# Kernel tuning notes

Measured on AMD Instinct MI355X. Metric: run time of the kernel, lower is better.

The kernel has to match this reference:

```python
import jax, jax.numpy as jnp
import numpy as np

EPS = 1e-12  # torch F.normalize eps


def setup_inputs() -> dict:
    key = jax.random.key(0)
    k1, k2, k3 = jax.random.split(key, 3)
    N, D, L = 8192, 768, 24576
    x = jax.random.normal(k1, (N, D), dtype=jnp.float32)
    # paper init: row-normalized gaussian rows of shape [latent_dim, input_dim]
    w = jax.random.normal(k2, (L, D), dtype=jnp.float32)
    enc_w = w / jnp.maximum(jnp.linalg.norm(w, axis=1, keepdims=True), EPS)
    enc_b = jax.random.normal(k3, (L,), dtype=jnp.float32) * 0.01
    pre_bias = jnp.zeros((D,), dtype=jnp.float32)
    return {"x": x, "enc_w": enc_w, "enc_b": enc_b, "pre_bias": pre_bias, "k": 32}


def _topk_mask(latents, k):
    # keep values >= k-th largest per row (ties kept, as in the torch code)
    vals, _ = jax.lax.top_k(latents, k)            # [N, k]
    thresh = vals[:, -1:]                          # [N, 1]
    return latents * (latents >= thresh)


def reference(x, enc_w, enc_b, pre_bias, k):
    # norm_input: subtract pre_bias then L2-normalize rows
    xc = x - pre_bias
    xn = xc / jnp.maximum(jnp.linalg.norm(xc, axis=1, keepdims=True), EPS)
    latents = xn @ enc_w.T + enc_b                 # [N, L]
    sparse = _topk_mask(latents, k)                # [N, L], ~k nonzeros/row
    # tied decoder: F.linear(sparse, enc_w.t()) == sparse @ enc_w
    out = sparse @ enc_w + pre_bias                # [N, D]
    return out, sparse
```

## Files before the change

### kernel.cpp

```cpp
#include <hip/hip_runtime.h>
#include <hip/hip_bf16.h>
#include <stdint.h>

#define N_ROWS 8192
#define DIM    768
#define LAT    24576
#define KSEL   32

using bf16x8 = __attribute__((ext_vector_type(8))) short;
using f32x4  = __attribute__((ext_vector_type(4))) float;

__device__ __forceinline__ unsigned short f2bf(float f) {
  unsigned int b = __float_as_uint(f);
  return (unsigned short)((b + 0x7FFFu + ((b >> 16) & 1u)) >> 16);
}
__device__ __forceinline__ float bf2f(unsigned short u) {
  return __uint_as_float(((unsigned int)u) << 16);
}
__device__ __forceinline__ unsigned int mapf(float f) {
  unsigned int u = __float_as_uint(f);
  return (u & 0x80000000u) ? ~u : (u | 0x80000000u);
}

__global__ __launch_bounds__(192) void k_norm(const float* __restrict__ x,
                                              const float* __restrict__ pre_bias,
                                              float* __restrict__ xn,
                                              unsigned short* __restrict__ xnbf) {
  const int row = blockIdx.x;
  const int t   = threadIdx.x;
  float4 xc = *(const float4*)&x[(size_t)row * DIM + t * 4];
  float4 pb = *(const float4*)&pre_bias[t * 4];
  xc.x -= pb.x; xc.y -= pb.y; xc.z -= pb.z; xc.w -= pb.w;
  double ss = (double)xc.x * xc.x + (double)xc.y * xc.y
            + (double)xc.z * xc.z + (double)xc.w * xc.w;
  #pragma unroll
  for (int off = 32; off; off >>= 1) ss += __shfl_down(ss, off);
  __shared__ double wsum[3];
  if ((t & 63) == 0) wsum[t >> 6] = ss;
  __syncthreads();
  const double tot = wsum[0] + wsum[1] + wsum[2];
  const float nrm = (float)fmax(sqrt(tot), 1e-12);
  float4 o;
  o.x = xc.x / nrm; o.y = xc.y / nrm; o.z = xc.z / nrm; o.w = xc.w / nrm;
  *(float4*)&xn[(size_t)row * DIM + t * 4] = o;
  if (xnbf) {
    ushort4 h;
    h.x = f2bf(o.x); h.y = f2bf(o.y); h.z = f2bf(o.z); h.w = f2bf(o.w);
    *(ushort4*)&xnbf[(size_t)row * DIM + t * 4] = h;
  }
}

__global__ __launch_bounds__(256) void k_cvt(const float* __restrict__ W,
                                             unsigned short* __restrict__ Wbf) {
  const int n4 = LAT * DIM / 4;
  const int stride = gridDim.x * blockDim.x;
  for (int i = blockIdx.x * blockDim.x + threadIdx.x; i < n4; i += stride) {
    float4 v = *(const float4*)&W[(size_t)i * 4];
    ushort4 h;
    h.x = f2bf(v.x); h.y = f2bf(v.y); h.z = f2bf(v.z); h.w = f2bf(v.w);
    *(ushort4*)&Wbf[(size_t)i * 4] = h;
  }
}

__global__ __launch_bounds__(256) void k_gemm_bf16(const unsigned short* __restrict__ A,
                                                   const unsigned short* __restrict__ B,
                                                   const float* __restrict__ bias,
                                                   unsigned short* __restrict__ C) {
  __shared__ __align__(16) unsigned short Al[2][128 * 32];
  __shared__ __align__(16) unsigned short Bl[2][128 * 32];
  const int tid  = threadIdx.x;
  const int lane = tid & 63;
  const int wave = tid >> 6;
  const int bm = blockIdx.y * 128;
  const int bn = blockIdx.x * 128;
  const int wr = (wave >> 1) * 64;
  const int wc = (wave & 1) * 64;
  const int fr = lane & 15;
  const int fq = lane >> 4;
  const int r0 = tid >> 2;
  const int c0 = tid & 3;

  f32x4 acc[4][4];
  #pragma unroll
  for (int m = 0; m < 4; ++m)
    #pragma unroll
    for (int n = 0; n < 4; ++n) acc[m][n] = (f32x4){0.f, 0.f, 0.f, 0.f};

  uint4 ra0, ra1, rb0, rb1;
  ra0 = *(const uint4*)&A[(size_t)(bm + r0) * DIM + c0 * 8];
  ra1 = *(const uint4*)&A[(size_t)(bm + 64 + r0) * DIM + c0 * 8];
  rb0 = *(const uint4*)&B[(size_t)(bn + r0) * DIM + c0 * 8];
  rb1 = *(const uint4*)&B[(size_t)(bn + 64 + r0) * DIM + c0 * 8];
  *(uint4*)&Al[0][r0 * 32 + c0 * 8]        = ra0;
  *(uint4*)&Al[0][(64 + r0) * 32 + c0 * 8] = ra1;
  *(uint4*)&Bl[0][r0 * 32 + c0 * 8]        = rb0;
  *(uint4*)&Bl[0][(64 + r0) * 32 + c0 * 8] = rb1;

  const int NT = DIM / 32;
  for (int kt = 0; kt < NT; ++kt) {
    const int buf = kt & 1;
    __syncthreads();
    if (kt + 1 < NT) {
      const int k0 = (kt + 1) * 32;
      ra0 = *(const uint4*)&A[(size_t)(bm + r0) * DIM + k0 + c0 * 8];
      ra1 = *(const uint4*)&A[(size_t)(bm + 64 + r0) * DIM + k0 + c0 * 8];
      rb0 = *(const uint4*)&B[(size_t)(bn + r0) * DIM + k0 + c0 * 8];
      rb1 = *(const uint4*)&B[(size_t)(bn + 64 + r0) * DIM + k0 + c0 * 8];
    }
    bf16x8 af[4], bfr[4];
    #pragma unroll
    for (int m = 0; m < 4; ++m)
      af[m] = *(const bf16x8*)&Al[buf][(wr + m * 16 + fr) * 32 + fq * 8];
    #pragma unroll
    for (int n = 0; n < 4; ++n)
      bfr[n] = *(const bf16x8*)&Bl[buf][(wc + n * 16 + fr) * 32 + fq * 8];
    #pragma unroll
    for (int m = 0; m < 4; ++m)
      #pragma unroll
      for (int n = 0; n < 4; ++n)
        acc[m][n] = __builtin_amdgcn_mfma_f32_16x16x32_bf16(af[m], bfr[n], acc[m][n], 0, 0, 0);
    if (kt + 1 < NT) {
      const int wb = buf ^ 1;
      *(uint4*)&Al[wb][r0 * 32 + c0 * 8]        = ra0;
      *(uint4*)&Al[wb][(64 + r0) * 32 + c0 * 8] = ra1;
      *(uint4*)&Bl[wb][r0 * 32 + c0 * 8]        = rb0;
      *(uint4*)&Bl[wb][(64 + r0) * 32 + c0 * 8] = rb1;
    }
  }

  #pragma unroll
  for (int n = 0; n < 4; ++n) {
    const int col = bn + wc + n * 16 + fr;
    const float bv = bias[col];
    #pragma unroll
    for (int m = 0; m < 4; ++m) {
      #pragma unroll
      for (int j = 0; j < 4; ++j) {
        const int row = bm + wr + m * 16 + fq * 4 + j;
        C[(size_t)row * LAT + col] = f2bf(acc[m][n][j] + bv);
      }
    }
  }
}

#define NBINS 8192
#define MARGIN 8e-3f
#define CCAP 192

__global__ __launch_bounds__(512) void k_screen(const unsigned short* __restrict__ S,
                                                int* __restrict__ cand_idx,
                                                int* __restrict__ cand_cnt) {
  const int row = blockIdx.x;
  const int t   = threadIdx.x;
  const unsigned short* rp = S + (size_t)row * LAT;

  float v[48];
  #pragma unroll
  for (int i = 0; i < 12; ++i) {
    ushort4 h = *(const ushort4*)&rp[(i * 512 + t) * 4];
    v[i * 4 + 0] = bf2f(h.x); v[i * 4 + 1] = bf2f(h.y);
    v[i * 4 + 2] = bf2f(h.z); v[i * 4 + 3] = bf2f(h.w);
  }

  __shared__ unsigned int hist[NBINS];
  __shared__ unsigned int csum[512];
  __shared__ unsigned int sh_chunk, sh_rchunk, sh_thru;
  __shared__ int sh_nc;
  if (t == 0) sh_nc = 0;
  #pragma unroll
  for (int i = 0; i < NBINS / 512; ++i) hist[t + i * 512] = 0u;
  __syncthreads();

  #pragma unroll
  for (int i = 0; i < 48; ++i) atomicAdd(&hist[mapf(v[i]) >> 19], 1u);
  __syncthreads();

  unsigned int cs = 0;
  #pragma unroll
  for (int i = 0; i < 16; ++i) cs += hist[t * 16 + i];
  csum[t] = cs;
  __syncthreads();
  for (int off = 1; off < 512; off <<= 1) {
    unsigned int add = (t + off < 512) ? csum[t + off] : 0u;
    __syncthreads();
    csum[t] += add;
    __syncthreads();
  }
  {
    const unsigned int nxt = (t + 1 < 512) ? csum[t + 1] : 0u;
    if (csum[t] >= KSEL && nxt < KSEL) { sh_chunk = (unsigned)t; sh_rchunk = nxt; }
  }
  __syncthreads();
  if (t == 0) {
    const unsigned int c0 = sh_chunk * 16u;
    unsigned int cum = sh_rchunk;
    unsigned int bin = c0;
    for (int b = 15; b >= 0; --b) {
      const unsigned int h = hist[c0 + b];
      if (cum + h >= KSEL) { bin = c0 + b; break; }
      cum += h;
    }
    const unsigned int lo = bin << 19;
    const unsigned int orig = (lo & 0x80000000u) ? (lo & 0x7FFFFFFFu) : ~lo;
    const float L = __uint_as_float(orig);
    sh_thru = mapf(L - MARGIN);
  }
  __syncthreads();
  const unsigned int thru = sh_thru;

  #pragma unroll
  for (int i = 0; i < 48; ++i) {
    if (mapf(v[i]) >= thru) {
      int p = atomicAdd(&sh_nc, 1);
      if (p < CCAP) cand_idx[row * CCAP + p] = ((i >> 2) * 512 + t) * 4 + (i & 3);
    }
  }
  __syncthreads();
  if (t == 0) cand_cnt[row] = (sh_nc < CCAP) ? sh_nc : CCAP;
}

__global__ __launch_bounds__(256) void k_rescore_seq(const float* __restrict__ xn,
                                                     const float* __restrict__ W,
                                                     const float* __restrict__ bias,
                                                     const int* __restrict__ cand_idx,
                                                     const int* __restrict__ cand_cnt,
                                                     float* __restrict__ tk_val,
                                                     int* __restrict__ tk_idx,
                                                     int* __restrict__ tk_cnt) {
  const int row = blockIdx.x;
  const int t   = threadIdx.x;
  const int cnt = cand_cnt[row];

  __shared__ float xs[DIM];
  __shared__ float rv[CCAP];
  __shared__ unsigned int sh_t;
  __shared__ int sh_kc;
  if (t == 0) sh_kc = 0;
  if (t < 192) *(float4*)&xs[t * 4] = *(const float4*)&xn[(size_t)row * DIM + t * 4];
  __syncthreads();

  if (t < cnt) {
    const int idx = cand_idx[row * CCAP + t];
    const float* wp = &W[(size_t)idx * DIM];
    float acc = 0.0f;
    for (int k4 = 0; k4 < DIM / 4; ++k4) {
      const float4 wv = *(const float4*)&wp[k4 * 4];
      acc = fmaf(xs[k4 * 4 + 0], wv.x, acc);
      acc = fmaf(xs[k4 * 4 + 1], wv.y, acc);
      acc = fmaf(xs[k4 * 4 + 2], wv.z, acc);
      acc = fmaf(xs[k4 * 4 + 3], wv.w, acc);
    }
    rv[t] = acc + bias[idx];
  }
  __syncthreads();

  if (t < cnt) {
    const unsigned int uj = mapf(rv[t]);
    unsigned int g = 0, ge = 0;
    for (int i = 0; i < cnt; ++i) {
      const unsigned int ui = mapf(rv[i]);
      g  += (ui >  uj);
      ge += (ui >= uj);
    }
    if (g < KSEL && ge >= KSEL) sh_t = uj;
  }
  __syncthreads();
  if (t < cnt) {
    const float val = rv[t];
    if (mapf(val) >= sh_t) {
      int p = atomicAdd(&sh_kc, 1);
      if (p < 64) { tk_val[row * 64 + p] = val; tk_idx[row * 64 + p] = cand_idx[row * CCAP + t]; }
    }
  }
  __syncthreads();
  if (t == 0) tk_cnt[row] = (sh_kc < 64) ? sh_kc : 64;
}

__global__ __launch_bounds__(256) void k_scatter(const float* __restrict__ tk_val,
                                                 const int* __restrict__ tk_idx,
                                                 const int* __restrict__ tk_cnt,
                                                 float* __restrict__ sparse) {
  const int row = blockIdx.x;
  const int t   = threadIdx.x;
  float* rp = sparse + (size_t)row * LAT;
  const float4 z = {0.f, 0.f, 0.f, 0.f};
  #pragma unroll
  for (int i = 0; i < LAT / (256 * 4); ++i) *(float4*)&rp[(i * 256 + t) * 4] = z;
  __syncthreads();
  if (t < tk_cnt[row]) rp[tk_idx[row * 64 + t]] = tk_val[row * 64 + t];
}

__global__ __launch_bounds__(192) void k_dec(const float* __restrict__ tk_val,
                                             const int* __restrict__ tk_idx,
                                             const int* __restrict__ tk_cnt,
                                             const float* __restrict__ W,
                                             const float* __restrict__ pre_bias,
                                             float* __restrict__ out) {
  const int row = blockIdx.x;
  const int t   = threadIdx.x;
  const int cnt = tk_cnt[row];
  float4 acc = *(const float4*)&pre_bias[t * 4];
  for (int e = 0; e < cnt; ++e) {
    const float val = tk_val[row * 64 + e];
    const int   idx = tk_idx[row * 64 + e];
    const float4 w = *(const float4*)&W[(size_t)idx * DIM + t * 4];
    acc.x = fmaf(val, w.x, acc.x);
    acc.y = fmaf(val, w.y, acc.y);
    acc.z = fmaf(val, w.z, acc.z);
    acc.w = fmaf(val, w.w, acc.w);
  }
  *(float4*)&out[(size_t)row * DIM + t * 4] = acc;
}

#define BM 128
#define BN 128
#define BK 32
#define PAD 4

__global__ __launch_bounds__(256) void k_gemm(const float* __restrict__ A,
                                              const float* __restrict__ B,
                                              const float* __restrict__ bias,
                                              float* __restrict__ C) {
  __shared__ float As[BK][BM + PAD];
  __shared__ float Bs[BK][BN + PAD];
  const int tid = threadIdx.x;
  const int bm = blockIdx.y * BM;
  const int bn = blockIdx.x * BN;
  const int tx = tid & 15;
  const int ty = tid >> 4;
  const int kq = tid & 7;
  const int rr = tid >> 3;

  float acc[8][8];
  #pragma unroll
  for (int i = 0; i < 8; ++i)
    #pragma unroll
    for (int j = 0; j < 8; ++j) acc[i][j] = 0.0f;

  float4 va[4], vb[4];
  #pragma unroll
  for (int i = 0; i < 4; ++i) {
    const int row = rr + 32 * i;
    va[i] = *(const float4*)&A[(size_t)(bm + row) * DIM + kq * 4];
    vb[i] = *(const float4*)&B[(size_t)(bn + row) * DIM + kq * 4];
  }

  for (int k0 = 0; k0 < DIM; k0 += BK) {
    #pragma unroll
    for (int i = 0; i < 4; ++i) {
      const int row = rr + 32 * i;
      As[kq * 4 + 0][row] = va[i].x; As[kq * 4 + 1][row] = va[i].y;
      As[kq * 4 + 2][row] = va[i].z; As[kq * 4 + 3][row] = va[i].w;
      Bs[kq * 4 + 0][row] = vb[i].x; Bs[kq * 4 + 1][row] = vb[i].y;
      Bs[kq * 4 + 2][row] = vb[i].z; Bs[kq * 4 + 3][row] = vb[i].w;
    }
    __syncthreads();
    if (k0 + BK < DIM) {
      #pragma unroll
      for (int i = 0; i < 4; ++i) {
        const int row = rr + 32 * i;
        va[i] = *(const float4*)&A[(size_t)(bm + row) * DIM + (k0 + BK) + kq * 4];
        vb[i] = *(const float4*)&B[(size_t)(bn + row) * DIM + (k0 + BK) + kq * 4];
      }
    }
    #pragma unroll
    for (int k = 0; k < BK; ++k) {
      float a[8], b[8];
      *(float4*)&b[0] = *(const float4*)&Bs[k][tx * 4];
      *(float4*)&b[4] = *(const float4*)&Bs[k][64 + tx * 4];
      *(float4*)&a[0] = *(const float4*)&As[k][ty * 8];
      *(float4*)&a[4] = *(const float4*)&As[k][ty * 8 + 4];
      #pragma unroll
      for (int i = 0; i < 8; ++i)
        #pragma unroll
        for (int j = 0; j < 8; ++j)
          acc[i][j] = fmaf(a[i], b[j], acc[i][j]);
    }
    __syncthreads();
  }

  const float4 b0 = *(const float4*)&bias[bn + tx * 4];
  const float4 b1 = *(const float4*)&bias[bn + 64 + tx * 4];
  #pragma unroll
  for (int i = 0; i < 8; ++i) {
    const size_t m = (size_t)(bm + ty * 8 + i);
    float4 v0, v1;
    v0.x = acc[i][0] + b0.x; v0.y = acc[i][1] + b0.y;
    v0.z = acc[i][2] + b0.z; v0.w = acc[i][3] + b0.w;
    v1.x = acc[i][4] + b1.x; v1.y = acc[i][5] + b1.y;
    v1.z = acc[i][6] + b1.z; v1.w = acc[i][7] + b1.w;
    *(float4*)&C[m * LAT + bn + tx * 4]      = v0;
    *(float4*)&C[m * LAT + bn + 64 + tx * 4] = v1;
  }
}

#define TPB_TK 512
#define CAND_CAP 512

template <int EMIT>
__global__ __launch_bounds__(TPB_TK) void k_topk(float* __restrict__ lat,
                                                 float* __restrict__ tk_val,
                                                 int* __restrict__ tk_idx,
                                                 int* __restrict__ tk_cnt) {
  const int row = blockIdx.x;
  const int t   = threadIdx.x;
  float* rowp = lat + (size_t)row * LAT;

  float4 v[12];
  #pragma unroll
  for (int i = 0; i < 12; ++i) v[i] = *(const float4*)&rowp[(i * TPB_TK + t) * 4];

  __shared__ unsigned int hist[NBINS];
  __shared__ unsigned int csum[TPB_TK];
  __shared__ unsigned int cand[CAND_CAP];
  __shared__ int sh_nc, sh_kc;
  __shared__ unsigned int sh_bin, sh_need, sh_thresh, sh_rchunk, sh_chunk;

  if (t == 0) { sh_nc = 0; sh_kc = 0; }
  #pragma unroll
  for (int i = 0; i < NBINS / TPB_TK; ++i) hist[t + i * TPB_TK] = 0u;
  __syncthreads();

  #pragma unroll
  for (int i = 0; i < 12; ++i) {
    atomicAdd(&hist[mapf(v[i].x) >> 19], 1u);
    atomicAdd(&hist[mapf(v[i].y) >> 19], 1u);
    atomicAdd(&hist[mapf(v[i].z) >> 19], 1u);
    atomicAdd(&hist[mapf(v[i].w) >> 19], 1u);
  }
  __syncthreads();

  unsigned int cs = 0;
  #pragma unroll
  for (int i = 0; i < 16; ++i) cs += hist[t * 16 + i];
  csum[t] = cs;
  __syncthreads();
  for (int off = 1; off < TPB_TK; off <<= 1) {
    unsigned int add = (t + off < TPB_TK) ? csum[t + off] : 0u;
    __syncthreads();
    csum[t] += add;
    __syncthreads();
  }
  {
    const unsigned int nxt = (t + 1 < TPB_TK) ? csum[t + 1] : 0u;
    if (csum[t] >= KSEL && nxt < KSEL) { sh_chunk = (unsigned)t; sh_rchunk = nxt; }
  }
  __syncthreads();
  if (t == 0) {
    const unsigned int c0 = sh_chunk * 16u;
    unsigned int cum = sh_rchunk;
    for (int b = 15; b >= 0; --b) {
      const unsigned int h = hist[c0 + b];
      if (cum + h >= KSEL) { sh_bin = c0 + b; sh_need = KSEL - cum; break; }
      cum += h;
    }
  }
  __syncthreads();
  const unsigned int bstar = sh_bin;

  #pragma unroll
  for (int i = 0; i < 12; ++i) {
    unsigned int u;
    u = mapf(v[i].x); if ((u >> 19) == bstar) { int p = atomicAdd(&sh_nc, 1); if (p < CAND_CAP) cand[p] = u; }
    u = mapf(v[i].y); if ((u >> 19) == bstar) { int p = atomicAdd(&sh_nc, 1); if (p < CAND_CAP) cand[p] = u; }
    u = mapf(v[i].z); if ((u >> 19) == bstar) { int p = atomicAdd(&sh_nc, 1); if (p < CAND_CAP) cand[p] = u; }
    u = mapf(v[i].w); if ((u >> 19) == bstar) { int p = atomicAdd(&sh_nc, 1); if (p < CAND_CAP) cand[p] = u; }
  }
  __syncthreads();
  const int nc = (sh_nc < CAND_CAP) ? sh_nc : CAND_CAP;
  const unsigned int need = sh_need;
  for (int j = t; j < nc; j += TPB_TK) {
    const unsigned int uj = cand[j];
    unsigned int g = 0, ge = 0;
    for (int i = 0; i < nc; ++i) {
      g  += (cand[i] >  uj);
      ge += (cand[i] >= uj);
    }
    if (g < need && ge >= need) sh_thresh = uj;
  }
  __syncthreads();
  const unsigned int tu = sh_thresh;

  #pragma unroll
  for (int i = 0; i < 12; ++i) {
    const int base = (i * TPB_TK + t) * 4;
    float4 o = v[i];
    unsigned int u;
    u = mapf(o.x); if (u >= tu) { if (EMIT) { int p = atomicAdd(&sh_kc, 1); if (p < 64) { tk_val[row * 64 + p] = o.x; tk_idx[row * 64 + p] = base + 0; } } } else o.x = 0.0f;
    u = mapf(o.y); if (u >= tu) { if (EMIT) { int p = atomicAdd(&sh_kc, 1); if (p < 64) { tk_val[row * 64 + p] = o.y; tk_idx[row * 64 + p] = base + 1; } } } else o.y = 0.0f;
    u = mapf(o.z); if (u >= tu) { if (EMIT) { int p = atomicAdd(&sh_kc, 1); if (p < 64) { tk_val[row * 64 + p] = o.z; tk_idx[row * 64 + p] = base + 2; } } } else o.z = 0.0f;
    u = mapf(o.w); if (u >= tu) { if (EMIT) { int p = atomicAdd(&sh_kc, 1); if (p < 64) { tk_val[row * 64 + p] = o.w; tk_idx[row * 64 + p] = base + 3; } } } else o.w = 0.0f;
    *(float4*)&rowp[base] = o;
  }
  if (EMIT) {
    __syncthreads();
    if (t == 0) tk_cnt[row] = (sh_kc < 64) ? sh_kc : 64;
  }
}

__global__ __launch_bounds__(256) void k_dec_scan(const float* __restrict__ sparse,
                                                  const float* __restrict__ W,
                                                  const float* __restrict__ pre_bias,
                                                  float* __restrict__ out) {
  const int row = blockIdx.x;
  const int t   = threadIdx.x;
  const float* rowp = sparse + (size_t)row * LAT;

  __shared__ float sval[96];
  __shared__ int   sidx[96];
  __shared__ int   scnt;
  if (t == 0) scnt = 0;
  __syncthreads();

  #pragma unroll
  for (int i = 0; i < LAT / (256 * 4); ++i) {
    const int base = (i * 256 + t) * 4;
    const float4 v = *(const float4*)&rowp[base];
    if (v.x != 0.0f) { int p = atomicAdd(&scnt, 1); if (p < 96) { sval[p] = v.x; sidx[p] = base + 0; } }
    if (v.y != 0.0f) { int p = atomicAdd(&scnt, 1); if (p < 96) { sval[p] = v.y; sidx[p] = base + 1; } }
    if (v.z != 0.0f) { int p = atomicAdd(&scnt, 1); if (p < 96) { sval[p] = v.z; sidx[p] = base + 2; } }
    if (v.w != 0.0f) { int p = atomicAdd(&scnt, 1); if (p < 96) { sval[p] = v.w; sidx[p] = base + 3; } }
  }
  __syncthreads();
  const int cnt = (scnt < 96) ? scnt : 96;

  if (t < 192) {
    float4 acc = *(const float4*)&pre_bias[t * 4];
    for (int e = 0; e < cnt; ++e) {
      const float val = sval[e];
      const float4 w = *(const float4*)&W[(size_t)sidx[e] * DIM + t * 4];
      acc.x = fmaf(val, w.x, acc.x);
      acc.y = fmaf(val, w.y, acc.y);
      acc.z = fmaf(val, w.z, acc.z);
      acc.w = fmaf(val, w.w, acc.w);
    }
    *(float4*)&out[(size_t)row * DIM + t * 4] = acc;
  }
}

extern "C" void kernel_launch(void* const* d_in, const int* in_sizes, int n_in,
                              void* d_out, int out_size, void* d_ws, size_t ws_size,
                              hipStream_t stream) {
  const float* x        = (const float*)d_in[0];
  const float* enc_w    = (const float*)d_in[1];
  const float* enc_b    = (const float*)d_in[2];
  const float* pre_bias = (const float*)d_in[3];

  float* out    = (float*)d_out;
  float* sparse = (float*)d_out + (size_t)N_ROWS * DIM;
  float* xn     = out;

  char* spb = (char*)sparse;
  unsigned short* xnbf   = (unsigned short*)spb;
  unsigned short* wbf    = (unsigned short*)(spb + (size_t)N_ROWS * DIM * 2);
  unsigned short* screen = (unsigned short*)(sparse + (size_t)N_ROWS * LAT / 2);

  char* wsb = (char*)d_ws;
  size_t off = 0;
  int*   cand_idx = (int*)(wsb + off); off += (size_t)N_ROWS * CCAP * 4;
  int*   cand_cnt = (int*)(wsb + off); off += (size_t)N_ROWS * 4;
  float* tk_val   = (float*)(wsb + off); off += (size_t)N_ROWS * 64 * 4;
  int*   tk_idx   = (int*)(wsb + off); off += (size_t)N_ROWS * 64 * 4;
  int*   tk_cnt   = (int*)(wsb + off); off += (size_t)N_ROWS * 4;
  const bool fast = ws_size >= off;

  if (fast) {
    k_norm<<<N_ROWS, 192, 0, stream>>>(x, pre_bias, xn, xnbf);
    k_cvt<<<2048, 256, 0, stream>>>(enc_w, wbf);
    dim3 ggrid(LAT / 128, N_ROWS / 128);
    k_gemm_bf16<<<ggrid, 256, 0, stream>>>(xnbf, wbf, enc_b, screen);
    k_screen<<<N_ROWS, 512, 0, stream>>>(screen, cand_idx, cand_cnt);
    k_rescore_seq<<<N_ROWS, 256, 0, stream>>>(xn, enc_w, enc_b, cand_idx, cand_cnt,
                                              tk_val, tk_idx, tk_cnt);
    k_scatter<<<N_ROWS, 256, 0, stream>>>(tk_val, tk_idx, tk_cnt, sparse);
    k_dec<<<N_ROWS, 192, 0, stream>>>(tk_val, tk_idx, tk_cnt, enc_w, pre_bias, out);
  } else {
    const size_t ws_small = (size_t)N_ROWS * 64 * 4 * 2 + (size_t)N_ROWS * 4;
    const bool use_lists = ws_size >= ws_small;
    float* f_val = (float*)d_ws;
    int*   f_idx = (int*)(f_val + (size_t)N_ROWS * 64);
    int*   f_cnt = f_idx + (size_t)N_ROWS * 64;

    k_norm<<<N_ROWS, 192, 0, stream>>>(x, pre_bias, xn, nullptr);
    dim3 ggrid(LAT / BN, N_ROWS / BM);
    k_gemm<<<ggrid, 256, 0, stream>>>(xn, enc_w, enc_b, sparse);
    if (use_lists) {
      k_topk<1><<<N_ROWS, TPB_TK, 0, stream>>>(sparse, f_val, f_idx, f_cnt);
      k_dec<<<N_ROWS, 192, 0, stream>>>(f_val, f_idx, f_cnt, enc_w, pre_bias, out);
    } else {
      k_topk<0><<<N_ROWS, TPB_TK, 0, stream>>>(sparse, nullptr, nullptr, nullptr);
      k_dec_scan<<<N_ROWS, 256, 0, stream>>>(sparse, enc_w, pre_bias, out);
    }
  }
}
```

Before: 1.797 ms.

## Use direct global-to-LDS loads in bf16 GEMM and fuse scatter with decoder

The bf16 screening GEMM now stages tiles with global_load_lds, which writes global data straight into LDS and skips the register round trip and explicit LDS stores. Each wave loads two 16-row segments, laid out so the LDS layout matches the old one. Separately, the scatter and decoder kernels are merged into one launch per row, saving a kernel launch and a reread of the top-k lists. The fp32 GEMM and top-k kernels are only moved within the file. The GEMM keeps a single barrier per iteration with no explicit wait on the async LDS loads, which could risk a race.

Result: no change. 1.810 ms (+0.7%).

```diff
diff --git a/kernel.cpp b/kernel.cpp
--- a/kernel.cpp
+++ b/kernel.cpp
@@ -20,6 +20,13 @@
 __device__ __forceinline__ unsigned int mapf(float f) {
   unsigned int u = __float_as_uint(f);
   return (u & 0x80000000u) ? ~u : (u | 0x80000000u);
+}
+
+__device__ __forceinline__ void gload16(const unsigned short* g, unsigned short* l) {
+  __builtin_amdgcn_global_load_lds(
+      (const __attribute__((address_space(1))) unsigned int*)(uintptr_t)g,
+      (__attribute__((address_space(3))) unsigned int*)(unsigned int)(uintptr_t)l,
+      16, 0, 0);
 }
 
 __global__ __launch_bounds__(192) void k_norm(const float* __restrict__ x,
@@ -77,8 +84,15 @@
   const int wc = (wave & 1) * 64;
   const int fr = lane & 15;
   const int fq = lane >> 4;
-  const int r0 = tid >> 2;
-  const int c0 = tid & 3;
+
+  const int seg0 = wave * 2;
+  const int rseg = lane >> 2;
+  const int ch   = lane & 3;
+
+  const unsigned short* gA0 = &A[(size_t)(bm + 16 * seg0 +      rseg) * DIM + ch * 8];
+  const unsigned short* gA1 = &A[(size_t)(bm + 16 * seg0 + 16 + rseg) * DIM + ch * 8];
+  const unsigned short* gB0 = &B[(size_t)(bn + 16 * seg0 +      rseg) * DIM + ch * 8];
+  const unsigned short* gB1 = &B[(size_t)(bn + 16 * seg0 + 16 + rseg) * DIM + ch * 8];
 
   f32x4 acc[4][4];
   #pragma unroll
@@ -86,27 +100,21 @@
     #pragma unroll
     for (int n = 0; n < 4; ++n) acc[m][n] = (f32x4){0.f, 0.f, 0.f, 0.f};
 
-  uint4 ra0, ra1, rb0, rb1;
-  ra0 = *(const uint4*)&A[(size_t)(bm + r0) * DIM + c0 * 8];
-  ra1 = *(const uint4*)&A[(size_t)(bm + 64 + r0) * DIM + c0 * 8];
-  rb0 = *(const uint4*)&B[(size_t)(bn + r0) * DIM + c0 * 8];
-  rb1 = *(const uint4*)&B[(size_t)(bn + 64 + r0) * DIM + c0 * 8];
-  *(uint4*)&Al[0][r0 * 32 + c0 * 8]        = ra0;
-  *(uint4*)&Al[0][(64 + r0) * 32 + c0 * 8] = ra1;
-  *(uint4*)&Bl[0][r0 * 32 + c0 * 8]        = rb0;
-  *(uint4*)&Bl[0][(64 + r0) * 32 + c0 * 8] = rb1;
+#define STAGE(buf, k0)                                            \
+  do {                                                            \
+    gload16(gA0 + (k0), &Al[buf][(seg0)     * 512]);              \
+    gload16(gA1 + (k0), &Al[buf][(seg0 + 1) * 512]);              \
+    gload16(gB0 + (k0), &Bl[buf][(seg0)     * 512]);              \
+    gload16(gB1 + (k0), &Bl[buf][(seg0 + 1) * 512]);              \
+  } while (0)
+
+  STAGE(0, 0);
 
   const int NT = DIM / 32;
   for (int kt = 0; kt < NT; ++kt) {
     const int buf = kt & 1;
     __syncthreads();
-    if (kt + 1 < NT) {
-      const int k0 = (kt + 1) * 32;
-      ra0 = *(const uint4*)&A[(size_t)(bm + r0) * DIM + k0 + c0 * 8];
-      ra1 = *(const uint4*)&A[(size_t)(bm + 64 + r0) * DIM + k0 + c0 * 8];
-      rb0 = *(const uint4*)&B[(size_t)(bn + r0) * DIM + k0 + c0 * 8];
-      rb1 = *(const uint4*)&B[(size_t)(bn + 64 + r0) * DIM + k0 + c0 * 8];
-    }
+    if (kt + 1 < NT) STAGE(buf ^ 1, (kt + 1) * 32);
     bf16x8 af[4], bfr[4];
     #pragma unroll
     for (int m = 0; m < 4; ++m)
@@ -119,14 +127,8 @@
       #pragma unroll
       for (int n = 0; n < 4; ++n)
         acc[m][n] = __builtin_amdgcn_mfma_f32_16x16x32_bf16(af[m], bfr[n], acc[m][n], 0, 0, 0);
-    if (kt + 1 < NT) {
-      const int wb = buf ^ 1;
-      *(uint4*)&Al[wb][r0 * 32 + c0 * 8]        = ra0;
-      *(uint4*)&Al[wb][(64 + r0) * 32 + c0 * 8] = ra1;
-      *(uint4*)&Bl[wb][r0 * 32 + c0 * 8]        = rb0;
-      *(uint4*)&Bl[wb][(64 + r0) * 32 + c0 * 8] = rb1;
-    }
-  }
+  }
+#undef STAGE
 
   #pragma unroll
   for (int n = 0; n < 4; ++n) {
@@ -276,10 +278,13 @@
   if (t == 0) tk_cnt[row] = (sh_kc < 64) ? sh_kc : 64;
 }
 
-__global__ __launch_bounds__(256) void k_scatter(const float* __restrict__ tk_val,
-                                                 const int* __restrict__ tk_idx,
-                                                 const int* __restrict__ tk_cnt,
-                                                 float* __restrict__ sparse) {
+__global__ __launch_bounds__(256) void k_scatter_dec(const float* __restrict__ tk_val,
+                                                     const int* __restrict__ tk_idx,
+                                                     const int* __restrict__ tk_cnt,
+                                                     const float* __restrict__ W,
+                                                     const float* __restrict__ pre_bias,
+                                                     float* __restrict__ sparse,
+                                                     float* __restrict__ out) {
   const int row = blockIdx.x;
   const int t   = threadIdx.x;
   float* rp = sparse + (size_t)row * LAT;
@@ -287,7 +292,207 @@
   #pragma unroll
   for (int i = 0; i < LAT / (256 * 4); ++i) *(float4*)&rp[(i * 256 + t) * 4] = z;
   __syncthreads();
-  if (t < tk_cnt[row]) rp[tk_idx[row * 64 + t]] = tk_val[row * 64 + t];
+  const int cnt = tk_cnt[row];
+  if (t < cnt) rp[tk_idx[row * 64 + t]] = tk_val[row * 64 + t];
+  if (t < 192) {
+    float4 acc = *(const float4*)&pre_bias[t * 4];
+    for (int e = 0; e < cnt; ++e) {
+      const float val = tk_val[row * 64 + e];
+      const int   idx = tk_idx[row * 64 + e];
+      const float4 w = *(const float4*)&W[(size_t)idx * DIM + t * 4];
+      acc.x = fmaf(val, w.x, acc.x);
+      acc.y = fmaf(val, w.y, acc.y);
+      acc.z = fmaf(val, w.z, acc.z);
+      acc.w = fmaf(val, w.w, acc.w);
+    }
+    *(float4*)&out[(size_t)row * DIM + t * 4] = acc;
+  }
+}
+
+#define BM 128
+#define BN 128
+#define BK 32
+#define PAD 4
+
+__global__ __launch_bounds__(256) void k_gemm(const float* __restrict__ A,
+                                              const float* __restrict__ B,
+                                              const float* __restrict__ bias,
+                                              float* __restrict__ C) {
+  __shared__ float As[BK][BM + PAD];
+  __shared__ float Bs[BK][BN + PAD];
+  const int tid = threadIdx.x;
+  const int bm = blockIdx.y * BM;
+  const int bn = blockIdx.x * BN;
+  const int tx = tid & 15;
+  const int ty = tid >> 4;
+  const int kq = tid & 7;
+  const int rr = tid >> 3;
+
+  float acc[8][8];
+  #pragma unroll
+  for (int i = 0; i < 8; ++i)
+    #pragma unroll
+    for (int j = 0; j < 8; ++j) acc[i][j] = 0.0f;
+
+  float4 va[4], vb[4];
+  #pragma unroll
+  for (int i = 0; i < 4; ++i) {
+    const int row = rr + 32 * i;
+    va[i] = *(const float4*)&A[(size_t)(bm + row) * DIM + kq * 4];
+    vb[i] = *(const float4*)&B[(size_t)(bn + row) * DIM + kq * 4];
+  }
+
+  for (int k0 = 0; k0 < DIM; k0 += BK) {
+    #pragma unroll
+    for (int i = 0; i < 4; ++i) {
+      const int row = rr + 32 * i;
+      As[kq * 4 + 0][row] = va[i].x; As[kq * 4 + 1][row] = va[i].y;
+      As[kq * 4 + 2][row] = va[i].z; As[kq * 4 + 3][row] = va[i].w;
+      Bs[kq * 4 + 0][row] = vb[i].x; Bs[kq * 4 + 1][row] = vb[i].y;
+      Bs[kq * 4 + 2][row] = vb[i].z; Bs[kq * 4 + 3][row] = vb[i].w;
+    }
+    __syncthreads();
+    if (k0 + BK < DIM) {
+      #pragma unroll
+      for (int i = 0; i < 4; ++i) {
+        const int row = rr + 32 * i;
+        va[i] = *(const float4*)&A[(size_t)(bm + row) * DIM + (k0 + BK) + kq * 4];
+        vb[i] = *(const float4*)&B[(size_t)(bn + row) * DIM + (k0 + BK) + kq * 4];
+      }
+    }
+    #pragma unroll
+    for (int k = 0; k < BK; ++k) {
+      float a[8], b[8];
+      *(float4*)&b[0] = *(const float4*)&Bs[k][tx * 4];
+      *(float4*)&b[4] = *(const float4*)&Bs[k][64 + tx * 4];
+      *(float4*)&a[0] = *(const float4*)&As[k][ty * 8];
+      *(float4*)&a[4] = *(const float4*)&As[k][ty * 8 + 4];
+      #pragma unroll
+      for (int i = 0; i < 8; ++i)
+        #pragma unroll
+        for (int j = 0; j < 8; ++j)
+          acc[i][j] = fmaf(a[i], b[j], acc[i][j]);
+    }
+    __syncthreads();
+  }
+
+  const float4 b0 = *(const float4*)&bias[bn + tx * 4];
+  const float4 b1 = *(const float4*)&bias[bn + 64 + tx * 4];
+  #pragma unroll
+  for (int i = 0; i < 8; ++i) {
+    const size_t m = (size_t)(bm + ty * 8 + i);
+    float4 v0, v1;
+    v0.x = acc[i][0] + b0.x; v0.y = acc[i][1] + b0.y;
+    v0.z = acc[i][2] + b0.z; v0.w = acc[i][3] + b0.w;
+    v1.x = acc[i][4] + b1.x; v1.y = acc[i][5] + b1.y;
+    v1.z = acc[i][6] + b1.z; v1.w = acc[i][7] + b1.w;
+    *(float4*)&C[m * LAT + bn + tx * 4]      = v0;
+    *(float4*)&C[m * LAT + bn + 64 + tx * 4] = v1;
+  }
+}
+
+#define TPB_TK 512
+#define CAND_CAP 512
+
+template <int EMIT>
+__global__ __launch_bounds__(TPB_TK) void k_topk(float* __restrict__ lat,
+                                                 float* __restrict__ tk_val,
+                                                 int* __restrict__ tk_idx,
+                                                 int* __restrict__ tk_cnt) {
+  const int row = blockIdx.x;
+  const int t   = threadIdx.x;
+  float* rowp = lat + (size_t)row * LAT;
+
+  float4 v[12];
+  #pragma unroll
+  for (int i = 0; i < 12; ++i) v[i] = *(const float4*)&rowp[(i * TPB_TK + t) * 4];
+
+  __shared__ unsigned int hist[NBINS];
+  __shared__ unsigned int csum[TPB_TK];
+  __shared__ unsigned int cand[CAND_CAP];
+  __shared__ int sh_nc, sh_kc;
+  __shared__ unsigned int sh_bin, sh_need, sh_thresh, sh_rchunk, sh_chunk;
+
+  if (t == 0) { sh_nc = 0; sh_kc = 0; }
+  #pragma unroll
+  for (int i = 0; i < NBINS / TPB_TK; ++i) hist[t + i * TPB_TK] = 0u;
+  __syncthreads();
+
+  #pragma unroll
+  for (int i = 0; i < 12; ++i) {
+    atomicAdd(&hist[mapf(v[i].x) >> 19], 1u);
+    atomicAdd(&hist[mapf(v[i].y) >> 19], 1u);
+    atomicAdd(&hist[mapf(v[i].z) >> 19], 1u);
+    atomicAdd(&hist[mapf(v[i].w) >> 19], 1u);
+  }
+  __syncthreads();
+
+  unsigned int cs = 0;
+  #pragma unroll
+  for (int i = 0; i < 16; ++i) cs += hist[t * 16 + i];
+  csum[t] = cs;
+  __syncthreads();
+  for (int off = 1; off < TPB_TK; off <<= 1) {
+    unsigned int add = (t + off < TPB_TK) ? csum[t + off] : 0u;
+    __syncthreads();
+    csum[t] += add;
+    __syncthreads();
+  }
+  {
+    const unsigned int nxt = (t + 1 < TPB_TK) ? csum[t + 1] : 0u;
+    if (csum[t] >= KSEL && nxt < KSEL) { sh_chunk = (unsigned)t; sh_rchunk = nxt; }
+  }
+  __syncthreads();
+  if (t == 0) {
+    const unsigned int c0 = sh_chunk * 16u;
+    unsigned int cum = sh_rchunk;
+    for (int b = 15; b >= 0; --b) {
+      const unsigned int h = hist[c0 + b];
+      if (cum + h >= KSEL) { sh_bin = c0 + b; sh_need = KSEL - cum; break; }
+      cum += h;
+    }
+  }
+  __syncthreads();
+  const unsigned int bstar = sh_bin;
+
+  #pragma unroll
+  for (int i = 0; i < 12; ++i) {
+    unsigned int u;
+    u = mapf(v[i].x); if ((u >> 19) == bstar) { int p = atomicAdd(&sh_nc, 1); if (p < CAND_CAP) cand[p] = u; }
+    u = mapf(v[i].y); if ((u >> 19) == bstar) { int p = atomicAdd(&sh_nc, 1); if (p < CAND_CAP) cand[p] = u; }
+    u = mapf(v[i].z); if ((u >> 19) == bstar) { int p = atomicAdd(&sh_nc, 1); if (p < CAND_CAP) cand[p] = u; }
+    u = mapf(v[i].w); if ((u >> 19) == bstar) { int p = atomicAdd(&sh_nc, 1); if (p < CAND_CAP) cand[p] = u; }
+  }
+  __syncthreads();
+  const int nc = (sh_nc < CAND_CAP) ? sh_nc : CAND_CAP;
+  const unsigned int need = sh_need;
+  for (int j = t; j < nc; j += TPB_TK) {
+    const unsigned int uj = cand[j];
+    unsigned int g = 0, ge = 0;
+    for (int i = 0; i < nc; ++i) {
+      g  += (cand[i] >  uj);
+      ge += (cand[i] >= uj);
+    }
+    if (g < need && ge >= need) sh_thresh = uj;
+  }
+  __syncthreads();
+  const unsigned int tu = sh_thresh;
+
+  #pragma unroll
+  for (int i = 0; i < 12; ++i) {
+    const int base = (i * TPB_TK + t) * 4;
+    float4 o = v[i];
+    unsigned int u;
+    u = mapf(o.x); if (u >= tu) { if (EMIT) { int p = atomicAdd(&sh_kc, 1); if (p < 64) { tk_val[row * 64 + p] = o.x; tk_idx[row * 64 + p] = base + 0; } } } else o.x = 0.0f;
+    u = mapf(o.y); if (u >= tu) { if (EMIT) { int p = atomicAdd(&sh_kc, 1); if (p < 64) { tk_val[row * 64 + p] = o.y; tk_idx[row * 64 + p] = base + 1; } } } else o.y = 0.0f;
+    u = mapf(o.z); if (u >= tu) { if (EMIT) { int p = atomicAdd(&sh_kc, 1); if (p < 64) { tk_val[row * 64 + p] = o.z; tk_idx[row * 64 + p] = base + 2; } } } else o.z = 0.0f;
+    u = mapf(o.w); if (u >= tu) { if (EMIT) { int p = atomicAdd(&sh_kc, 1); if (p < 64) { tk_val[row * 64 + p] = o.w; tk_idx[row * 64 + p] = base + 3; } } } else o.w = 0.0f;
+    *(float4*)&rowp[base] = o;
+  }
+  if (EMIT) {
+    __syncthreads();
+    if (t == 0) tk_cnt[row] = (sh_kc < 64) ? sh_kc : 64;
+  }
 }
 
 __global__ __launch_bounds__(192) void k_dec(const float* __restrict__ tk_val,
@@ -312,192 +517,6 @@
   *(float4*)&out[(size_t)row * DIM + t * 4] = acc;
 }
 
-#define BM 128
-#define BN 128
-#define BK 32
-#define PAD 4
-
-__global__ __launch_bounds__(256) void k_gemm(const float* __restrict__ A,
-                                              const float* __restrict__ B,
-                                              const float* __restrict__ bias,
-                                              float* __restrict__ C) {
-  __shared__ float As[BK][BM + PAD];
-  __shared__ float Bs[BK][BN + PAD];
-  const int tid = threadIdx.x;
-  const int bm = blockIdx.y * BM;
-  const int bn = blockIdx.x * BN;
-  const int tx = tid & 15;
-  const int ty = tid >> 4;
-  const int kq = tid & 7;
-  const int rr = tid >> 3;
-
-  float acc[8][8];
-  #pragma unroll
-  for (int i = 0; i < 8; ++i)
-    #pragma unroll
-    for (int j = 0; j < 8; ++j) acc[i][j] = 0.0f;
-
-  float4 va[4], vb[4];
-  #pragma unroll
-  for (int i = 0; i < 4; ++i) {
-    const int row = rr + 32 * i;
-    va[i] = *(const float4*)&A[(size_t)(bm + row) * DIM + kq * 4];
-    vb[i] = *(const float4*)&B[(size_t)(bn + row) * DIM + kq * 4];
-  }
-
-  for (int k0 = 0; k0 < DIM; k0 += BK) {
-    #pragma unroll
-    for (int i = 0; i < 4; ++i) {
-      const int row = rr + 32 * i;
-      As[kq * 4 + 0][row] = va[i].x; As[kq * 4 + 1][row] = va[i].y;
-      As[kq * 4 + 2][row] = va[i].z; As[kq * 4 + 3][row] = va[i].w;
-      Bs[kq * 4 + 0][row] = vb[i].x; Bs[kq * 4 + 1][row] = vb[i].y;
-      Bs[kq * 4 + 2][row] = vb[i].z; Bs[kq * 4 + 3][row] = vb[i].w;
-    }
-    __syncthreads();
-    if (k0 + BK < DIM) {
-      #pragma unroll
-      for (int i = 0; i < 4; ++i) {
-        const int row = rr + 32 * i;
-        va[i] = *(const float4*)&A[(size_t)(bm + row) * DIM + (k0 + BK) + kq * 4];
-        vb[i] = *(const float4*)&B[(size_t)(bn + row) * DIM + (k0 + BK) + kq * 4];
-      }
-    }
-    #pragma unroll
-    for (int k = 0; k < BK; ++k) {
-      float a[8], b[8];
-      *(float4*)&b[0] = *(const float4*)&Bs[k][tx * 4];
-      *(float4*)&b[4] = *(const float4*)&Bs[k][64 + tx * 4];
-      *(float4*)&a[0] = *(const float4*)&As[k][ty * 8];
-      *(float4*)&a[4] = *(const float4*)&As[k][ty * 8 + 4];
-      #pragma unroll
-      for (int i = 0; i < 8; ++i)
-        #pragma unroll
-        for (int j = 0; j < 8; ++j)
-          acc[i][j] = fmaf(a[i], b[j], acc[i][j]);
-    }
-    __syncthreads();
-  }
-
-  const float4 b0 = *(const float4*)&bias[bn + tx * 4];
-  const float4 b1 = *(const float4*)&bias[bn + 64 + tx * 4];
-  #pragma unroll
-  for (int i = 0; i < 8; ++i) {
-    const size_t m = (size_t)(bm + ty * 8 + i);
-    float4 v0, v1;
-    v0.x = acc[i][0] + b0.x; v0.y = acc[i][1] + b0.y;
-    v0.z = acc[i][2] + b0.z; v0.w = acc[i][3] + b0.w;
-    v1.x = acc[i][4] + b1.x; v1.y = acc[i][5] + b1.y;
-    v1.z = acc[i][6] + b1.z; v1.w = acc[i][7] + b1.w;
-    *(float4*)&C[m * LAT + bn + tx * 4]      = v0;
-    *(float4*)&C[m * LAT + bn + 64 + tx * 4] = v1;
-  }
-}
-
-#define TPB_TK 512
-#define CAND_CAP 512
-
-template <int EMIT>
-__global__ __launch_bounds__(TPB_TK) void k_topk(float* __restrict__ lat,
-                                                 float* __restrict__ tk_val,
-                                                 int* __restrict__ tk_idx,
-                                                 int* __restrict__ tk_cnt) {
-  const int row = blockIdx.x;
-  const int t   = threadIdx.x;
-  float* rowp = lat + (size_t)row * LAT;
-
-  float4 v[12];
-  #pragma unroll
-  for (int i = 0; i < 12; ++i) v[i] = *(const float4*)&rowp[(i * TPB_TK + t) * 4];
-
-  __shared__ unsigned int hist[NBINS];
-  __shared__ unsigned int csum[TPB_TK];
-  __shared__ unsigned int cand[CAND_CAP];
-  __shared__ int sh_nc, sh_kc;
-  __shared__ unsigned int sh_bin, sh_need, sh_thresh, sh_rchunk, sh_chunk;
-
-  if (t == 0) { sh_nc = 0; sh_kc = 0; }
-  #pragma unroll
-  for (int i = 0; i < NBINS / TPB_TK; ++i) hist[t + i * TPB_TK] = 0u;
-  __syncthreads();
-
-  #pragma unroll
-  for (int i = 0; i < 12; ++i) {
-    atomicAdd(&hist[mapf(v[i].x) >> 19], 1u);
-    atomicAdd(&hist[mapf(v[i].y) >> 19], 1u);
-    atomicAdd(&hist[mapf(v[i].z) >> 19], 1u);
-    atomicAdd(&hist[mapf(v[i].w) >> 19], 1u);
-  }
-  __syncthreads();
-
-  unsigned int cs = 0;
-  #pragma unroll
-  for (int i = 0; i < 16; ++i) cs += hist[t * 16 + i];
-  csum[t] = cs;
-  __syncthreads();
-  for (int off = 1; off < TPB_TK; off <<= 1) {
-    unsigned int add = (t + off < TPB_TK) ? csum[t + off] : 0u;
-    __syncthreads();
-    csum[t] += add;
-    __syncthreads();
-  }
-  {
-    const unsigned int nxt = (t + 1 < TPB_TK) ? csum[t + 1] : 0u;
-    if (csum[t] >= KSEL && nxt < KSEL) { sh_chunk = (unsigned)t; sh_rchunk = nxt; }
-  }
-  __syncthreads();
-  if (t == 0) {
-    const unsigned int c0 = sh_chunk * 16u;
-    unsigned int cum = sh_rchunk;
-    for (int b = 15; b >= 0; --b) {
-      const unsigned int h = hist[c0 + b];
-      if (cum + h >= KSEL) { sh_bin = c0 + b; sh_need = KSEL - cum; break; }
-      cum += h;
-    }
-  }
-  __syncthreads();
-  const unsigned int bstar = sh_bin;
-
-  #pragma unroll
-  for (int i = 0; i < 12; ++i) {
-    unsigned int u;
-    u = mapf(v[i].x); if ((u >> 19) == bstar) { int p = atomicAdd(&sh_nc, 1); if (p < CAND_CAP) cand[p] = u; }
-    u = mapf(v[i].y); if ((u >> 19) == bstar) { int p = atomicAdd(&sh_nc, 1); if (p < CAND_CAP) cand[p] = u; }
-    u = mapf(v[i].z); if ((u >> 19) == bstar) { int p = atomicAdd(&sh_nc, 1); if (p < CAND_CAP) cand[p] = u; }
-    u = mapf(v[i].w); if ((u >> 19) == bstar) { int p = atomicAdd(&sh_nc, 1); if (p < CAND_CAP) cand[p] = u; }
-  }
-  __syncthreads();
-  const int nc = (sh_nc < CAND_CAP) ? sh_nc : CAND_CAP;
-  const unsigned int need = sh_need;
-  for (int j = t; j < nc; j += TPB_TK) {
-    const unsigned int uj = cand[j];
-    unsigned int g = 0, ge = 0;
-    for (int i = 0; i < nc; ++i) {
-      g  += (cand[i] >  uj);
-      ge += (cand[i] >= uj);
-    }
-    if (g < need && ge >= need) sh_thresh = uj;
-  }
-  __syncthreads();
-  const unsigned int tu = sh_thresh;
-
-  #pragma unroll
-  for (int i = 0; i < 12; ++i) {
-    const int base = (i * TPB_TK + t) * 4;
-    float4 o = v[i];
-    unsigned int u;
-    u = mapf(o.x); if (u >= tu) { if (EMIT) { int p = atomicAdd(&sh_kc, 1); if (p < 64) { tk_val[row * 64 + p] = o.x; tk_idx[row * 64 + p] = base + 0; } } } else o.x = 0.0f;
-    u = mapf(o.y); if (u >= tu) { if (EMIT) { int p = atomicAdd(&sh_kc, 1); if (p < 64) { tk_val[row * 64 + p] = o.y; tk_idx[row * 64 + p] = base + 1; } } } else o.y = 0.0f;
-    u = mapf(o.z); if (u >= tu) { if (EMIT) { int p = atomicAdd(&sh_kc, 1); if (p < 64) { tk_val[row * 64 + p] = o.z; tk_idx[row * 64 + p] = base + 2; } } } else o.z = 0.0f;
-    u = mapf(o.w); if (u >= tu) { if (EMIT) { int p = atomicAdd(&sh_kc, 1); if (p < 64) { tk_val[row * 64 + p] = o.w; tk_idx[row * 64 + p] = base + 3; } } } else o.w = 0.0f;
-    *(float4*)&rowp[base] = o;
-  }
-  if (EMIT) {
-    __syncthreads();
-    if (t == 0) tk_cnt[row] = (sh_kc < 64) ? sh_kc : 64;
-  }
-}
-
 __global__ __launch_bounds__(256) void k_dec_scan(const float* __restrict__ sparse,
                                                   const float* __restrict__ W,
                                                   const float* __restrict__ pre_bias,
@@ -572,8 +591,8 @@
     k_screen<<<N_ROWS, 512, 0, stream>>>(screen, cand_idx, cand_cnt);
     k_rescore_seq<<<N_ROWS, 256, 0, stream>>>(xn, enc_w, enc_b, cand_idx, cand_cnt,
                                               tk_val, tk_idx, tk_cnt);
-    k_scatter<<<N_ROWS, 256, 0, stream>>>(tk_val, tk_idx, tk_cnt, sparse);
-    k_dec<<<N_ROWS, 192, 0, stream>>>(tk_val, tk_idx, tk_cnt, enc_w, pre_bias, out);
+    k_scatter_dec<<<N_ROWS, 256, 0, stream>>>(tk_val, tk_idx, tk_cnt, enc_w, pre_bias,
+                                              sparse, out);
   } else {
     const size_t ws_small = (size_t)N_ROWS * 64 * 4 * 2 + (size_t)N_ROWS * 4;
     const bool use_lists = ws_size >= ws_small;
```
